# Kernel tuning notes

Measured on AMD Instinct MI355X. Metric: run time of the kernel, lower is better.

Reference implementation:

```python
import jax, jax.numpy as jnp
import numpy as np

N_NODES = 100_000
N_EDGES = 3_200_000
FAN_IN, FAN_MID, FAN_OUT = 512, 256, 64
NEG_SLOPE = 0.01  # F.leaky_relu default


def setup_inputs() -> dict:
    key = jax.random.key(0)
    ks = jax.random.split(key, 8)
    x = jax.random.normal(ks[0], (N_NODES, FAN_IN), dtype=jnp.float32)
    edge_src = jax.random.randint(ks[1], (N_EDGES,), 0, N_NODES, dtype=jnp.int32)
    edge_dst = jax.random.randint(ks[2], (N_EDGES,), 0, N_NODES, dtype=jnp.int32)
    edge_w1 = jax.random.uniform(ks[3], (N_EDGES,), dtype=jnp.float32)
    edge_w2 = jax.random.uniform(ks[4], (N_EDGES,), dtype=jnp.float32)
    W1 = jax.random.normal(ks[5], (FAN_IN, FAN_MID), dtype=jnp.float32) * (1.0 / np.sqrt(FAN_IN))
    b1 = jnp.zeros((FAN_MID,), dtype=jnp.float32)
    W2 = jax.random.normal(ks[6], (FAN_MID, FAN_OUT), dtype=jnp.float32) * (1.0 / np.sqrt(FAN_MID))
    b2 = jnp.zeros((FAN_OUT,), dtype=jnp.float32)
    return {"x": x, "edge_src": edge_src, "edge_dst": edge_dst,
            "edge_w1": edge_w1, "edge_w2": edge_w2,
            "W1": W1, "b1": b1, "W2": W2, "b2": b2}


def _gcn_layer(x, W, b, src, dst, ew):
    # GraphConvolution: support = x @ W ; out = A @ support + b (A sparse via edges)
    support = x @ W                                 # [N, F_out]
    msgs = support[src] * ew[:, None]               # gather + scale, [E, F_out]
    agg = jax.ops.segment_sum(msgs, dst, num_segments=x.shape[0])  # scatter-add
    return agg + b


def reference(x, edge_src, edge_dst, edge_w1, edge_w2, W1, b1, W2, b2):
    h = _gcn_layer(x, W1, b1, edge_src, edge_dst, edge_w1)
    h = jax.nn.leaky_relu(h, NEG_SLOPE)
    # dropout is identity at inference (training=False)
    h = _gcn_layer(h, W2, b2, edge_src, edge_dst, edge_w2)
    return jax.nn.log_softmax(h, axis=1)
```

## Files before the change

### kernel.cpp

```cpp
#include <hip/hip_runtime.h>
#include <stdint.h>

#define FAN_IN  512
#define FAN_MID 256
#define FAN_OUT 64
#define NEG_SLOPE 0.01f
#define NPB 128
#define MAXNB 1024
#define BPART 256

typedef __bf16 bf16_t;
typedef bf16_t bf16x8 __attribute__((ext_vector_type(8)));
typedef float  f32x4  __attribute__((ext_vector_type(4)));
typedef unsigned short u16x8 __attribute__((ext_vector_type(8)));

__device__ inline unsigned short f2b(float f) {
    union { float f; unsigned int u; } v; v.f = f;
    unsigned int u = v.u;
    return (unsigned short)((u + 0x7fffu + ((u >> 16) & 1u)) >> 16);
}
__device__ inline float b2f(unsigned short u) {
    union { unsigned int u; float f; } v; v.u = ((unsigned int)u) << 16; return v.f;
}

__global__ void zerob_kernel(int* p, int n) {
    int i = blockIdx.x * 256 + threadIdx.x;
    if (i < n) p[i] = 0;
}

__global__ __launch_bounds__(256) void part_hist(const int* __restrict__ dst,
                                                 int* __restrict__ gcount,
                                                 int* __restrict__ bcount,
                                                 int E, int nb, int chunk) {
    __shared__ int lc[MAXNB];
    int blk = blockIdx.x;
    for (int i = threadIdx.x; i < nb; i += 256) lc[i] = 0;
    __syncthreads();
    int s = blk * chunk;
    int e = s + chunk; if (e > E) e = E;
    for (int i = s + threadIdx.x; i < e; i += 256)
        atomicAdd(&lc[dst[i] >> 7], 1);
    __syncthreads();
    for (int i = threadIdx.x; i < nb; i += 256) {
        int c = lc[i];
        gcount[blk * nb + i] = c;
        if (c) atomicAdd(&bcount[i], c);
    }
}

__global__ void bscan_kernel(const int* __restrict__ bcount, int* __restrict__ boff,
                             int nb, int E) {
    __shared__ int part[1024];
    int t = threadIdx.x;
    int chunk = (nb + 1023) >> 10;
    int s = t * chunk;
    int e = s + chunk; if (e > nb) e = nb;
    int sum = 0;
    for (int i = s; i < e; i++) sum += bcount[i];
    part[t] = sum;
    __syncthreads();
    for (int off = 1; off < 1024; off <<= 1) {
        int v = (t >= off) ? part[t - off] : 0;
        __syncthreads();
        part[t] += v;
        __syncthreads();
    }
    int run = (t == 0) ? 0 : part[t - 1];
    for (int i = s; i < e; i++) {
        boff[i] = run;
        run += bcount[i];
    }
    if (t == 1023) boff[nb] = E;
}

__global__ __launch_bounds__(BPART) void part_scan(const int* __restrict__ gcount,
                                                   const int* __restrict__ boff,
                                                   int* __restrict__ gbase, int nb) {
    __shared__ int v[BPART];
    int bucket = blockIdx.x;
    int t = threadIdx.x;
    int val = gcount[t * nb + bucket];
    v[t] = val;
    __syncthreads();
    for (int off = 1; off < BPART; off <<= 1) {
        int x = (t >= off) ? v[t - off] : 0;
        __syncthreads();
        v[t] += x;
        __syncthreads();
    }
    gbase[t * nb + bucket] = (t == 0 ? 0 : v[t - 1]) + boff[bucket];
}

__global__ __launch_bounds__(256) void part_scatter(const int* __restrict__ src,
                                                    const int* __restrict__ dst,
                                                    const float* __restrict__ w1,
                                                    const float* __restrict__ w2,
                                                    const int* __restrict__ gbase,
                                                    uint4* __restrict__ bstage,
                                                    int E, int nb, int chunk) {
    __shared__ int lcur[MAXNB];
    int blk = blockIdx.x;
    for (int i = threadIdx.x; i < nb; i += 256) lcur[i] = gbase[blk * nb + i];
    __syncthreads();
    int s = blk * chunk;
    int e = s + chunk; if (e > E) e = E;
    for (int i = s + threadIdx.x; i < e; i += 256) {
        int d = dst[i];
        int pos = atomicAdd(&lcur[d >> 7], 1);
        uint4 v;
        v.x = (unsigned int)src[i];
        v.y = __float_as_uint(w1[i]);
        v.z = __float_as_uint(w2[i]);
        v.w = (unsigned int)d;
        bstage[pos] = v;
    }
}

__global__ __launch_bounds__(256) void bsort_kernel(const uint4* __restrict__ bstage,
                                                    const int* __restrict__ boff,
                                                    int* __restrict__ offsets,
                                                    uint2* __restrict__ csr1,
                                                    uint2* __restrict__ csr2,
                                                    int Nn, int E, int nb) {
    __shared__ int cnt[NPB];
    __shared__ int scn[NPB];
    __shared__ int cur[NPB];
    int b = blockIdx.x;
    int t = threadIdx.x;
    int base = boff[b], end = boff[b + 1];
    int n0 = b * NPB;
    if (t < NPB) cnt[t] = 0;
    __syncthreads();
    for (int i = base + t; i < end; i += 256)
        atomicAdd(&cnt[bstage[i].w - n0], 1);
    __syncthreads();
    if (t == 0) {
        int run = 0;
        for (int j = 0; j < NPB; j++) { scn[j] = run; run += cnt[j]; }
    }
    __syncthreads();
    if (t < NPB) {
        cur[t] = scn[t];
        int n = n0 + t;
        if (n < Nn) offsets[n] = base + scn[t];
    }
    if (b == nb - 1 && t == 0) offsets[Nn] = E;
    __syncthreads();
    for (int i = base + t; i < end; i += 256) {
        uint4 rec = bstage[i];
        int lp = atomicAdd(&cur[rec.w - n0], 1);
        uint2 r1; r1.x = rec.x; r1.y = rec.y;
        uint2 r2; r2.x = rec.x; r2.y = rec.z;
        csr1[base + lp] = r1;
        csr2[base + lp] = r2;
    }
}

__global__ void convert_w_kernel(const float* __restrict__ W, unsigned short* __restrict__ Wt,
                                 int K, int N) {
    int idx = blockIdx.x * 256 + threadIdx.x;
    if (idx >= K * N) return;
    int k = idx / N, n = idx % N;
    Wt[(size_t)n * K + k] = f2b(W[idx]);
}

template<int K, int N, bool A_F32>
__global__ __launch_bounds__(256) void gemm_bt(const void* __restrict__ Ap,
                                               const unsigned short* __restrict__ Bt,
                                               unsigned short* __restrict__ C, int M) {
    constexpr int LDT = 40;
    constexpr int NW  = N / 64;
    __shared__ unsigned short As[64 * LDT];
    __shared__ unsigned short Bs[N * LDT];
    const int m0   = blockIdx.x * 64;
    const int tid  = threadIdx.x;
    const int lane = tid & 63;
    const int w    = tid >> 6;
    const int lrow = tid >> 2;
    const int lseg = (tid & 3) * 8;
    const int q    = lane >> 4;
    const int mm   = lane & 15;

    f32x4 acc[4][NW] = {};

    for (int k0 = 0; k0 < K; k0 += 32) {
        __syncthreads();
        {
            int gm = m0 + lrow;
            u16x8 av;
            if (A_F32) {
                const float* A32 = (const float*)Ap;
                if (gm < M) {
                    const float4* pp = (const float4*)(A32 + (size_t)gm * K + k0 + lseg);
                    float4 f0 = pp[0], f1 = pp[1];
                    av[0] = f2b(f0.x); av[1] = f2b(f0.y); av[2] = f2b(f0.z); av[3] = f2b(f0.w);
                    av[4] = f2b(f1.x); av[5] = f2b(f1.y); av[6] = f2b(f1.z); av[7] = f2b(f1.w);
                } else av = (u16x8)0;
            } else {
                const unsigned short* A16 = (const unsigned short*)Ap;
                if (gm < M) av = *(const u16x8*)(A16 + (size_t)gm * K + k0 + lseg);
                else        av = (u16x8)0;
            }
            *(u16x8*)&As[lrow * LDT + lseg] = av;
        }
#pragma unroll
        for (int r = 0; r < N / 64; r++) {
            int nr = r * 64 + lrow;
            *(u16x8*)&Bs[nr * LDT + lseg] =
                *(const u16x8*)(Bt + (size_t)nr * K + k0 + lseg);
        }
        __syncthreads();

        bf16x8 a[4], b[NW];
#pragma unroll
        for (int mi = 0; mi < 4; mi++)
            a[mi] = *(const bf16x8*)&As[(mi * 16 + mm) * LDT + q * 8];
#pragma unroll
        for (int ni = 0; ni < NW; ni++)
            b[ni] = *(const bf16x8*)&Bs[(w * NW * 16 + ni * 16 + mm) * LDT + q * 8];
#pragma unroll
        for (int mi = 0; mi < 4; mi++)
#pragma unroll
            for (int ni = 0; ni < NW; ni++)
                acc[mi][ni] = __builtin_amdgcn_mfma_f32_16x16x32_bf16(a[mi], b[ni], acc[mi][ni], 0, 0, 0);
    }

#pragma unroll
    for (int mi = 0; mi < 4; mi++)
#pragma unroll
        for (int ni = 0; ni < NW; ni++)
#pragma unroll
            for (int r = 0; r < 4; r++) {
                int row = m0 + mi * 16 + q * 4 + r;
                if (row < M)
                    C[(size_t)row * N + w * NW * 16 + ni * 16 + mm] = f2b(acc[mi][ni][r]);
            }
}

__global__ __launch_bounds__(256) void agg1_kernel(const unsigned short* __restrict__ S,
                                                   const int* __restrict__ offsets,
                                                   const uint2* __restrict__ edges,
                                                   const float* __restrict__ b1,
                                                   unsigned short* __restrict__ h, int Nn) {
    int wave = threadIdx.x >> 6;
    int lane = threadIdx.x & 63;
    int node = blockIdx.x * 4 + wave;
    if (node >= Nn) return;
    int s = offsets[node], e = offsets[node + 1];
    float a0 = 0.f, a1 = 0.f, a2 = 0.f, a3 = 0.f;
    int i = s;
    for (; i + 8 <= e; i += 8) {
        uint2 ed[8];
#pragma unroll
        for (int j = 0; j < 8; j++) ed[j] = edges[i + j];
        ushort4 v[8];
#pragma unroll
        for (int j = 0; j < 8; j++)
            v[j] = *(const ushort4*)(S + (size_t)ed[j].x * 256 + lane * 4);
#pragma unroll
        for (int j = 0; j < 8; j++) {
            float w = __uint_as_float(ed[j].y);
            a0 += w * b2f(v[j].x);
            a1 += w * b2f(v[j].y);
            a2 += w * b2f(v[j].z);
            a3 += w * b2f(v[j].w);
        }
    }
    for (; i + 4 <= e; i += 4) {
        uint2 ed[4];
#pragma unroll
        for (int j = 0; j < 4; j++) ed[j] = edges[i + j];
        ushort4 v[4];
#pragma unroll
        for (int j = 0; j < 4; j++)
            v[j] = *(const ushort4*)(S + (size_t)ed[j].x * 256 + lane * 4);
#pragma unroll
        for (int j = 0; j < 4; j++) {
            float w = __uint_as_float(ed[j].y);
            a0 += w * b2f(v[j].x);
            a1 += w * b2f(v[j].y);
            a2 += w * b2f(v[j].z);
            a3 += w * b2f(v[j].w);
        }
    }
    for (; i < e; i++) {
        uint2 ev = edges[i];
        float w = __uint_as_float(ev.y);
        ushort4 v = *(const ushort4*)(S + (size_t)ev.x * 256 + lane * 4);
        a0 += w * b2f(v.x); a1 += w * b2f(v.y); a2 += w * b2f(v.z); a3 += w * b2f(v.w);
    }
    float4 bb = ((const float4*)b1)[lane];
    float r0 = a0 + bb.x, r1 = a1 + bb.y, r2 = a2 + bb.z, r3 = a3 + bb.w;
    r0 = r0 > 0.f ? r0 : r0 * NEG_SLOPE;
    r1 = r1 > 0.f ? r1 : r1 * NEG_SLOPE;
    r2 = r2 > 0.f ? r2 : r2 * NEG_SLOPE;
    r3 = r3 > 0.f ? r3 : r3 * NEG_SLOPE;
    ushort4 o;
    o.x = f2b(r0); o.y = f2b(r1); o.z = f2b(r2); o.w = f2b(r3);
    *(ushort4*)&h[(size_t)node * 256 + lane * 4] = o;
}

__global__ __launch_bounds__(256) void agg2_kernel(const unsigned short* __restrict__ S,
                                                   const int* __restrict__ offsets,
                                                   const uint2* __restrict__ edges,
                                                   const float* __restrict__ b2,
                                                   float* __restrict__ out, int Nn) {
    int wave = threadIdx.x >> 6;
    int lane = threadIdx.x & 63;
    int node = blockIdx.x * 4 + wave;
    if (node >= Nn) return;
    int s = offsets[node], e = offsets[node + 1];
    float acc = 0.f;
    int i = s;
    for (; i + 8 <= e; i += 8) {
        uint2 ed[8];
#pragma unroll
        for (int j = 0; j < 8; j++) ed[j] = edges[i + j];
        float v[8];
#pragma unroll
        for (int j = 0; j < 8; j++)
            v[j] = b2f(S[(size_t)ed[j].x * 64 + lane]);
#pragma unroll
        for (int j = 0; j < 8; j++)
            acc += __uint_as_float(ed[j].y) * v[j];
    }
    for (; i + 4 <= e; i += 4) {
        uint2 ed[4];
#pragma unroll
        for (int j = 0; j < 4; j++) ed[j] = edges[i + j];
        float v[4];
#pragma unroll
        for (int j = 0; j < 4; j++)
            v[j] = b2f(S[(size_t)ed[j].x * 64 + lane]);
#pragma unroll
        for (int j = 0; j < 4; j++)
            acc += __uint_as_float(ed[j].y) * v[j];
    }
    for (; i < e; i++) {
        uint2 ev = edges[i];
        acc += __uint_as_float(ev.y) * b2f(S[(size_t)ev.x * 64 + lane]);
    }
    float logit = acc + b2[lane];
    float m = logit;
    for (int off = 32; off; off >>= 1) m = fmaxf(m, __shfl_xor(m, off));
    float ex = expf(logit - m);
    float sum = ex;
    for (int off = 32; off; off >>= 1) sum += __shfl_xor(sum, off);
    out[(size_t)node * 64 + lane] = logit - m - logf(sum);
}

extern "C" void kernel_launch(void* const* d_in, const int* in_sizes, int n_in,
                              void* d_out, int out_size, void* d_ws, size_t ws_size,
                              hipStream_t stream) {
    const float* x    = (const float*)d_in[0];
    const int*   esrc = (const int*)d_in[1];
    const int*   edst = (const int*)d_in[2];
    const float* ew1  = (const float*)d_in[3];
    const float* ew2  = (const float*)d_in[4];
    const float* W1   = (const float*)d_in[5];
    const float* b1   = (const float*)d_in[6];
    const float* W2   = (const float*)d_in[7];
    const float* b2   = (const float*)d_in[8];
    float* out = (float*)d_out;
    const int Nn = in_sizes[0] / FAN_IN;
    const int E  = in_sizes[1];
    const int NB = (Nn + NPB - 1) / NPB;
    const int chunk = (E + BPART - 1) / BPART;

    char* p = (char*)d_ws;
    auto alloc = [&](size_t bytes) -> char* {
        char* r = p;
        p += (bytes + 255) & ~(size_t)255;
        return r;
    };
    size_t s1_bytes = (size_t)Nn * FAN_MID * 2;
    size_t st_bytes = (size_t)E * 16;
    char* s1_region = alloc(s1_bytes > st_bytes ? s1_bytes : st_bytes);
    unsigned short* support1 = (unsigned short*)s1_region;
    uint4*          bstage   = (uint4*)s1_region;
    unsigned short* h        = (unsigned short*)alloc((size_t)Nn * FAN_MID * 2);
    unsigned short* support2 = (unsigned short*)alloc((size_t)Nn * FAN_OUT * 2);
    unsigned short* W1t      = (unsigned short*)alloc((size_t)FAN_IN * FAN_MID * 2);
    unsigned short* W2t      = (unsigned short*)alloc((size_t)FAN_MID * FAN_OUT * 2);
    int*            bcount   = (int*)alloc((size_t)NB * 4);
    int*            boff     = (int*)alloc(((size_t)NB + 1) * 4);
    int*            gcount   = (int*)alloc((size_t)BPART * NB * 4);
    int*            gbase    = (int*)alloc((size_t)BPART * NB * 4);
    int*            offsets  = (int*)alloc(((size_t)Nn + 1) * 4);
    uint2*          csr1     = (uint2*)alloc((size_t)E * 8);
    uint2*          csr2     = (uint2*)alloc((size_t)E * 8);

    zerob_kernel<<<(NB + 255) / 256, 256, 0, stream>>>(bcount, NB);
    part_hist<<<BPART, 256, 0, stream>>>(edst, gcount, bcount, E, NB, chunk);
    bscan_kernel<<<1, 1024, 0, stream>>>(bcount, boff, NB, E);
    part_scan<<<NB, BPART, 0, stream>>>(gcount, boff, gbase, NB);
    part_scatter<<<BPART, 256, 0, stream>>>(esrc, edst, ew1, ew2, gbase, bstage, E, NB, chunk);
    bsort_kernel<<<NB, 256, 0, stream>>>(bstage, boff, offsets, csr1, csr2, Nn, E, NB);

    convert_w_kernel<<<(FAN_IN * FAN_MID + 255) / 256, 256, 0, stream>>>(W1, W1t, FAN_IN, FAN_MID);
    convert_w_kernel<<<(FAN_MID * FAN_OUT + 255) / 256, 256, 0, stream>>>(W2, W2t, FAN_MID, FAN_OUT);

    gemm_bt<FAN_IN, FAN_MID, true><<<dim3((Nn + 63) / 64, 1), 256, 0, stream>>>(
        x, W1t, support1, Nn);
    agg1_kernel<<<(Nn + 3) / 4, 256, 0, stream>>>(support1, offsets, csr1, b1, h, Nn);

    gemm_bt<FAN_MID, FAN_OUT, false><<<dim3((Nn + 63) / 64, 1), 256, 0, stream>>>(
        h, W2t, support2, Nn);
    agg2_kernel<<<(Nn + 3) / 4, 256, 0, stream>>>(support2, offsets, csr2, b2, out, Nn);
}
```

Measured before the change: 859.6 us.

## Split wave lanes across multiple edges with 16-byte gathers in both aggregation kernels

Both aggregation kernels now map lanes so a wave processes several edges at once. In agg1 each half-wave takes a different edge and loads 8 bf16 per lane. In agg2 eight 8-lane groups each take a different edge and load 16 bytes per lane, instead of one 2-byte load per lane per edge. The partial sums are combined with cross-lane shuffles before the bias, activation and log-softmax, and the stores are vectorised. This aims to cut the number of memory instructions and raise memory-level parallelism in the gather-bound kernels, at the cost of extra shuffles and more registers.

```diff
diff --git a/kernel.cpp b/kernel.cpp
--- a/kernel.cpp
+++ b/kernel.cpp
@@ -247,57 +247,57 @@
     int node = blockIdx.x * 4 + wave;
     if (node >= Nn) return;
     int s = offsets[node], e = offsets[node + 1];
-    float a0 = 0.f, a1 = 0.f, a2 = 0.f, a3 = 0.f;
+    const int half = lane >> 5;
+    const int elo  = lane & 31;
+    float acc[8] = {0.f, 0.f, 0.f, 0.f, 0.f, 0.f, 0.f, 0.f};
     int i = s;
-    for (; i + 8 <= e; i += 8) {
+    for (; i + 16 <= e; i += 16) {
         uint2 ed[8];
 #pragma unroll
-        for (int j = 0; j < 8; j++) ed[j] = edges[i + j];
-        ushort4 v[8];
-#pragma unroll
-        for (int j = 0; j < 8; j++)
-            v[j] = *(const ushort4*)(S + (size_t)ed[j].x * 256 + lane * 4);
-#pragma unroll
-        for (int j = 0; j < 8; j++) {
-            float w = __uint_as_float(ed[j].y);
-            a0 += w * b2f(v[j].x);
-            a1 += w * b2f(v[j].y);
-            a2 += w * b2f(v[j].z);
-            a3 += w * b2f(v[j].w);
+        for (int p = 0; p < 8; p++) ed[p] = edges[i + 2 * p + half];
+        u16x8 v[8];
+#pragma unroll
+        for (int p = 0; p < 8; p++)
+            v[p] = *(const u16x8*)(S + (size_t)ed[p].x * 256 + elo * 8);
+#pragma unroll
+        for (int p = 0; p < 8; p++) {
+            float w = __uint_as_float(ed[p].y);
+#pragma unroll
+            for (int k = 0; k < 8; k++) acc[k] += w * b2f(v[p][k]);
         }
     }
-    for (; i + 4 <= e; i += 4) {
-        uint2 ed[4];
-#pragma unroll
-        for (int j = 0; j < 4; j++) ed[j] = edges[i + j];
-        ushort4 v[4];
-#pragma unroll
-        for (int j = 0; j < 4; j++)
-            v[j] = *(const ushort4*)(S + (size_t)ed[j].x * 256 + lane * 4);
-#pragma unroll
-        for (int j = 0; j < 4; j++) {
-            float w = __uint_as_float(ed[j].y);
-            a0 += w * b2f(v[j].x);
-            a1 += w * b2f(v[j].y);
-            a2 += w * b2f(v[j].z);
-            a3 += w * b2f(v[j].w);
+    for (; i + 2 <= e; i += 2) {
+        uint2 ev = edges[i + half];
+        float w = __uint_as_float(ev.y);
+        u16x8 v = *(const u16x8*)(S + (size_t)ev.x * 256 + elo * 8);
+#pragma unroll
+        for (int k = 0; k < 8; k++) acc[k] += w * b2f(v[k]);
+    }
+    if (i < e) {
+        uint2 ev = edges[i];
+        float w = half ? 0.f : __uint_as_float(ev.y);
+        u16x8 v = *(const u16x8*)(S + (size_t)ev.x * 256 + elo * 8);
+#pragma unroll
+        for (int k = 0; k < 8; k++) acc[k] += w * b2f(v[k]);
+    }
+#pragma unroll
+    for (int k = 0; k < 8; k++) acc[k] += __shfl_xor(acc[k], 32);
+    if (half == 0) {
+        float4 bb0 = ((const float4*)b1)[elo * 2];
+        float4 bb1 = ((const float4*)b1)[elo * 2 + 1];
+        float r[8];
+        r[0] = acc[0] + bb0.x; r[1] = acc[1] + bb0.y;
+        r[2] = acc[2] + bb0.z; r[3] = acc[3] + bb0.w;
+        r[4] = acc[4] + bb1.x; r[5] = acc[5] + bb1.y;
+        r[6] = acc[6] + bb1.z; r[7] = acc[7] + bb1.w;
+        u16x8 o;
+#pragma unroll
+        for (int k = 0; k < 8; k++) {
+            float t = r[k] > 0.f ? r[k] : r[k] * NEG_SLOPE;
+            o[k] = f2b(t);
         }
-    }
-    for (; i < e; i++) {
-        uint2 ev = edges[i];
-        float w = __uint_as_float(ev.y);
-        ushort4 v = *(const ushort4*)(S + (size_t)ev.x * 256 + lane * 4);
-        a0 += w * b2f(v.x); a1 += w * b2f(v.y); a2 += w * b2f(v.z); a3 += w * b2f(v.w);
-    }
-    float4 bb = ((const float4*)b1)[lane];
-    float r0 = a0 + bb.x, r1 = a1 + bb.y, r2 = a2 + bb.z, r3 = a3 + bb.w;
-    r0 = r0 > 0.f ? r0 : r0 * NEG_SLOPE;
-    r1 = r1 > 0.f ? r1 : r1 * NEG_SLOPE;
-    r2 = r2 > 0.f ? r2 : r2 * NEG_SLOPE;
-    r3 = r3 > 0.f ? r3 : r3 * NEG_SLOPE;
-    ushort4 o;
-    o.x = f2b(r0); o.y = f2b(r1); o.z = f2b(r2); o.w = f2b(r3);
-    *(ushort4*)&h[(size_t)node * 256 + lane * 4] = o;
+        *(u16x8*)&h[(size_t)node * 256 + elo * 8] = o;
+    }
 }
 
 __global__ __launch_bounds__(256) void agg2_kernel(const unsigned short* __restrict__ S,
@@ -310,43 +310,71 @@
     int node = blockIdx.x * 4 + wave;
     if (node >= Nn) return;
     int s = offsets[node], e = offsets[node + 1];
-    float acc = 0.f;
+    const int slot = lane >> 3;
+    const int fblk = lane & 7;
+    float acc[8] = {0.f, 0.f, 0.f, 0.f, 0.f, 0.f, 0.f, 0.f};
     int i = s;
+    for (; i + 16 <= e; i += 16) {
+        uint2 e0 = edges[i + slot];
+        uint2 e1 = edges[i + 8 + slot];
+        u16x8 v0 = *(const u16x8*)(S + (size_t)e0.x * 64 + fblk * 8);
+        u16x8 v1 = *(const u16x8*)(S + (size_t)e1.x * 64 + fblk * 8);
+        float w0 = __uint_as_float(e0.y), w1 = __uint_as_float(e1.y);
+#pragma unroll
+        for (int k = 0; k < 8; k++) acc[k] += w0 * b2f(v0[k]) + w1 * b2f(v1[k]);
+    }
     for (; i + 8 <= e; i += 8) {
-        uint2 ed[8];
-#pragma unroll
-        for (int j = 0; j < 8; j++) ed[j] = edges[i + j];
-        float v[8];
-#pragma unroll
-        for (int j = 0; j < 8; j++)
-            v[j] = b2f(S[(size_t)ed[j].x * 64 + lane]);
-#pragma unroll
-        for (int j = 0; j < 8; j++)
-            acc += __uint_as_float(ed[j].y) * v[j];
-    }
-    for (; i + 4 <= e; i += 4) {
-        uint2 ed[4];
-#pragma unroll
-        for (int j = 0; j < 4; j++) ed[j] = edges[i + j];
-        float v[4];
-#pragma unroll
-        for (int j = 0; j < 4; j++)
-            v[j] = b2f(S[(size_t)ed[j].x * 64 + lane]);
-#pragma unroll
-        for (int j = 0; j < 4; j++)
-            acc += __uint_as_float(ed[j].y) * v[j];
-    }
-    for (; i < e; i++) {
-        uint2 ev = edges[i];
-        acc += __uint_as_float(ev.y) * b2f(S[(size_t)ev.x * 64 + lane]);
-    }
-    float logit = acc + b2[lane];
-    float m = logit;
-    for (int off = 32; off; off >>= 1) m = fmaxf(m, __shfl_xor(m, off));
-    float ex = expf(logit - m);
-    float sum = ex;
-    for (int off = 32; off; off >>= 1) sum += __shfl_xor(sum, off);
-    out[(size_t)node * 64 + lane] = logit - m - logf(sum);
+        uint2 ev = edges[i + slot];
+        u16x8 v = *(const u16x8*)(S + (size_t)ev.x * 64 + fblk * 8);
+        float w = __uint_as_float(ev.y);
+#pragma unroll
+        for (int k = 0; k < 8; k++) acc[k] += w * b2f(v[k]);
+    }
+    int rem = e - i;
+    if (rem > 0) {
+        int j = i + (slot < rem ? slot : rem - 1);
+        uint2 ev = edges[j];
+        float w = (slot < rem) ? __uint_as_float(ev.y) : 0.f;
+        u16x8 v = *(const u16x8*)(S + (size_t)ev.x * 64 + fblk * 8);
+#pragma unroll
+        for (int k = 0; k < 8; k++) acc[k] += w * b2f(v[k]);
+    }
+#pragma unroll
+    for (int k = 0; k < 8; k++) {
+        acc[k] += __shfl_xor(acc[k], 8);
+        acc[k] += __shfl_xor(acc[k], 16);
+        acc[k] += __shfl_xor(acc[k], 32);
+    }
+    float4 bb0 = ((const float4*)b2)[fblk * 2];
+    float4 bb1 = ((const float4*)b2)[fblk * 2 + 1];
+    float logit[8];
+    logit[0] = acc[0] + bb0.x; logit[1] = acc[1] + bb0.y;
+    logit[2] = acc[2] + bb0.z; logit[3] = acc[3] + bb0.w;
+    logit[4] = acc[4] + bb1.x; logit[5] = acc[5] + bb1.y;
+    logit[6] = acc[6] + bb1.z; logit[7] = acc[7] + bb1.w;
+    float m = logit[0];
+#pragma unroll
+    for (int k = 1; k < 8; k++) m = fmaxf(m, logit[k]);
+    m = fmaxf(m, __shfl_xor(m, 1));
+    m = fmaxf(m, __shfl_xor(m, 2));
+    m = fmaxf(m, __shfl_xor(m, 4));
+    float sum = 0.f;
+#pragma unroll
+    for (int k = 0; k < 8; k++) sum += expf(logit[k] - m);
+    sum += __shfl_xor(sum, 1);
+    sum += __shfl_xor(sum, 2);
+    sum += __shfl_xor(sum, 4);
+    float ls = logf(sum);
+    if (slot == 0) {
+        float* op = out + (size_t)node * 64 + fblk * 8;
+        float4 o0, o1;
+        o0.x = logit[0] - m - ls; o0.y = logit[1] - m - ls;
+        o0.z = logit[2] - m - ls; o0.w = logit[3] - m - ls;
+        o1.x = logit[4] - m - ls; o1.y = logit[5] - m - ls;
+        o1.z = logit[6] - m - ls; o1.w = logit[7] - m - ls;
+        ((float4*)op)[0] = o0;
+        ((float4*)op)[1] = o1;
+    }
 }
 
 extern "C" void kernel_launch(void* const* d_in, const int* in_sizes, int n_in,
```

After: 829.6 us. 3.5% less time.
